# Performance work log

Measured on AMD Instinct MI355X. Metric: run time of the kernel, lower is better.

Reference implementation:

```python
import jax, jax.numpy as jnp
import numpy as np

ROPE_BASE = 10000.0

def _rope_tables(T, head_dim, dtype):
    inv_freq = 1.0 / (ROPE_BASE ** (jnp.arange(0, head_dim, 2, dtype=jnp.float32) / head_dim))
    t = jnp.arange(T, dtype=jnp.float32)
    freqs = jnp.einsum('t,f->tf', t, inv_freq)          # [T, head_dim/2]
    emb = jnp.concatenate([freqs, freqs], axis=-1)       # [T, head_dim]
    return jnp.sin(emb).astype(dtype), jnp.cos(emb).astype(dtype)

def _rotate_half(x):
    d = x.shape[-1] // 2
    return jnp.concatenate([-x[..., d:], x[..., :d]], axis=-1)

def _apply_rotary(x, sin, cos):
    # x: [B,H,T,hd]; sin/cos: [T,hd] broadcast over B,H
    return x * cos + _rotate_half(x) * sin

def setup_inputs() -> dict:
    key = jax.random.key(0)
    k1, k2, k3 = jax.random.split(key, 3)
    B, T, E = 2, 2048, 2048
    x = jax.random.normal(k1, (B, T, E), dtype=jnp.float32)
    attention_mask = jnp.ones((B, T), dtype=jnp.int32)
    W_qkv = jax.random.normal(k2, (E, 3 * E), dtype=jnp.float32) * (E ** -0.5)
    W_proj = jax.random.normal(k3, (E, E), dtype=jnp.float32) * (E ** -0.5)
    return {"x": x, "attention_mask": attention_mask, "W_qkv": W_qkv, "W_proj": W_proj}

def reference(x, attention_mask, W_qkv, W_proj):
    B, T, E = x.shape
    H = 16
    hd = E // H
    qkv = (x @ W_qkv).reshape(B, T, 3, H, hd)
    q, k, v = (jnp.moveaxis(qkv[:, :, i], 1, 2) for i in range(3))  # each [B,H,T,hd]
    sin, cos = _rope_tables(T, hd, x.dtype)
    q = _apply_rotary(q, sin, cos)
    k = _apply_rotary(k, sin, cos)
    # mask: True = masked out (causal future, padded keys, padded queries)
    causal = jnp.triu(jnp.ones((T, T), dtype=bool), 1)[None, None]      # [1,1,T,T]
    pad_k = (attention_mask == 0)[:, None, None, :]                     # [B,1,1,T]
    pad_q = (attention_mask == 0)[:, None, :, None]                     # [B,1,T,1]
    mask = causal | pad_k | pad_q                                       # [B,1,T,T]
    scale = hd ** -0.5
    scores = jnp.einsum('bhqd,bhkd->bhqk', q, k) * scale
    scores = jnp.where(mask, jnp.asarray(-1e9, scores.dtype), scores)
    attn = jax.nn.softmax(scores, axis=-1)
    out = jnp.einsum('bhqk,bhkd->bhqd', attn, v)                        # [B,H,T,hd]
    out = jnp.moveaxis(out, 1, 2).reshape(B, T, E)
    return out @ W_proj
```

## Files before the change

kernel.cpp:

```cpp
#include <hip/hip_runtime.h>
#include <math.h>

#define TT 2048
#define EE 2048
#define NH 16
#define HD 128
#define MM 4096
#define GK 2048

using f32x4  = __attribute__((ext_vector_type(4))) float;
using bf16x8 = __attribute__((ext_vector_type(8))) short;

#define MFMA16(a, b, c) __builtin_amdgcn_mfma_f32_16x16x32_bf16(a, b, c, 0, 0, 0)

__device__ __forceinline__ ushort bf_hi(float x) {
    uint u = __float_as_uint(x);
    uint r = (u + 0x7fffu + ((u >> 16) & 1u)) >> 16;
    return (ushort)r;
}
__device__ __forceinline__ float bf_f(ushort h) {
    return __uint_as_float(((uint)h) << 16);
}

__device__ __forceinline__ void gload16(const void* g, void* l) {
    __builtin_amdgcn_global_load_lds((const __attribute__((address_space(1))) void*)g,
                                     (__attribute__((address_space(3))) void*)l, 16, 0, 0);
}


template <int MODE>
__global__ __launch_bounds__(256)
void gemm_k(const float* __restrict__ A, const float* __restrict__ B,
            float* __restrict__ o0, float* __restrict__ o1, float* __restrict__ o2,
            int M, int N, int K)
{
    __shared__ float As[16][132];
    __shared__ float Bs[16][132];

    const int tid = threadIdx.x;
    const int tx = tid & 15;
    const int ty = tid >> 4;
    const int bm = blockIdx.y * 128;
    const int bn = blockIdx.x * 128;

    const int arow = tid >> 2;
    const int acq  = (tid & 3) << 2;
    const int brow = tid >> 5;
    const int bcol = (tid & 31) << 2;

    const float* Aptr = A + (size_t)(bm + arow) * K + acq;
    const float* Bptr = B + (size_t)brow * N + bn + bcol;

    float acc[8][8];
#pragma unroll
    for (int i = 0; i < 8; ++i)
#pragma unroll
        for (int j = 0; j < 8; ++j) acc[i][j] = 0.f;

    for (int kt = 0; kt < K; kt += 16) {
        float4 a0 = *(const float4*)(Aptr + kt);
        float4 a1 = *(const float4*)(Aptr + kt + (size_t)64 * K);
        float4 b0 = *(const float4*)(Bptr + (size_t)kt * N);
        float4 b1 = *(const float4*)(Bptr + (size_t)(kt + 8) * N);
        __syncthreads();
        As[acq + 0][arow] = a0.x; As[acq + 1][arow] = a0.y;
        As[acq + 2][arow] = a0.z; As[acq + 3][arow] = a0.w;
        As[acq + 0][arow + 64] = a1.x; As[acq + 1][arow + 64] = a1.y;
        As[acq + 2][arow + 64] = a1.z; As[acq + 3][arow + 64] = a1.w;
        *(float4*)&Bs[brow][bcol]     = b0;
        *(float4*)&Bs[brow + 8][bcol] = b1;
        __syncthreads();
#pragma unroll
        for (int kk = 0; kk < 16; ++kk) {
            float4 a_0 = *(const float4*)&As[kk][ty * 8];
            float4 a_1 = *(const float4*)&As[kk][ty * 8 + 4];
            float4 b_0 = *(const float4*)&Bs[kk][tx * 4];
            float4 b_1 = *(const float4*)&Bs[kk][tx * 4 + 64];
            float ar[8] = {a_0.x, a_0.y, a_0.z, a_0.w, a_1.x, a_1.y, a_1.z, a_1.w};
            float br[8] = {b_0.x, b_0.y, b_0.z, b_0.w, b_1.x, b_1.y, b_1.z, b_1.w};
#pragma unroll
            for (int i = 0; i < 8; ++i)
#pragma unroll
                for (int j = 0; j < 8; ++j)
                    acc[i][j] = fmaf(ar[i], br[j], acc[i][j]);
        }
    }

    if (MODE == 0) {
#pragma unroll
        for (int i = 0; i < 8; ++i) {
            size_t rowoff = (size_t)(bm + ty * 8 + i) * N + bn;
            *(float4*)&o0[rowoff + tx * 4]      = make_float4(acc[i][0], acc[i][1], acc[i][2], acc[i][3]);
            *(float4*)&o0[rowoff + 64 + tx * 4] = make_float4(acc[i][4], acc[i][5], acc[i][6], acc[i][7]);
        }
    } else {
        const int sel = bn >> 11;
        const int h   = (bn & 2047) >> 7;
        float* dst = (sel == 0) ? o0 : ((sel == 1) ? o1 : o2);
#pragma unroll
        for (int i = 0; i < 8; ++i) {
            int m = bm + ty * 8 + i;
            int b = m >> 11;
            int t = m & 2047;
            size_t base = (((size_t)b * NH + h) * TT + t) * HD;
            *(float4*)&dst[base + tx * 4]      = make_float4(acc[i][0], acc[i][1], acc[i][2], acc[i][3]);
            *(float4*)&dst[base + 64 + tx * 4] = make_float4(acc[i][4], acc[i][5], acc[i][6], acc[i][7]);
        }
    }
}

__global__ __launch_bounds__(256)
void split_x(const float* __restrict__ x, ushort* __restrict__ xh,
             ushort* __restrict__ xl)
{
    int idx = (blockIdx.x * 256 + threadIdx.x) * 4;
    float4 v = *(const float4*)&x[idx];
    float f[4] = {v.x, v.y, v.z, v.w};
    ushort h[4], l[4];
#pragma unroll
    for (int e = 0; e < 4; ++e) {
        h[e] = bf_hi(f[e]);
        l[e] = bf_hi(f[e] - bf_f(h[e]));
    }
    *(ushort4*)&xh[idx] = make_ushort4(h[0], h[1], h[2], h[3]);
    *(ushort4*)&xl[idx] = make_ushort4(l[0], l[1], l[2], l[3]);
}

__global__ __launch_bounds__(256)
void tw_prep(const float* __restrict__ W, int ldw, int c0,
             ushort* __restrict__ th, ushort* __restrict__ tl)
{
    __shared__ float tile[32][33];
    const int k0 = blockIdx.x * 32, n0 = blockIdx.y * 32;
    const int tx = threadIdx.x & 31, ty = threadIdx.x >> 5;
#pragma unroll
    for (int j = 0; j < 4; ++j)
        tile[ty + 8 * j][tx] = W[(size_t)(k0 + ty + 8 * j) * ldw + c0 + n0 + tx];
    __syncthreads();
#pragma unroll
    for (int j = 0; j < 4; ++j) {
        float v = tile[tx][ty + 8 * j];
        ushort h = bf_hi(v);
        ushort l = bf_hi(v - bf_f(h));
        size_t off = (size_t)(n0 + ty + 8 * j) * GK + k0 + tx;
        th[off] = h;
        tl[off] = l;
    }
}

template <int SCATTER>
__global__ __launch_bounds__(256)
void gemm_bf16(const ushort* __restrict__ Ah, const ushort* __restrict__ Al,
               const ushort* __restrict__ Bh, const ushort* __restrict__ Bl,
               float* __restrict__ out)
{
    __shared__ ushort AhS[4096], AlS[4096], BhS[4096], BlS[4096];

    const int tid  = threadIdx.x;
    const int wid  = tid >> 6;
    const int lane = tid & 63;
    const int lh   = lane >> 4;
    const int j16  = lane & 15;
    const int wm   = wid >> 1, wn = wid & 1;
    const int bm   = blockIdx.y * 128, bn = blockIdx.x * 128;

    const int g0 = wid * 128 + lane;
    const int g1 = g0 + 64;
    const int r0 = g0 >> 2, o0 = (g0 & 3) ^ (r0 & 3);
    const int r1 = g1 >> 2, o1 = (g1 & 3) ^ (r1 & 3);
    const size_t sa0 = (size_t)(bm + r0) * GK + o0 * 8;
    const size_t sa1 = (size_t)(bm + r1) * GK + o1 * 8;
    const size_t sb0 = (size_t)(bn + r0) * GK + o0 * 8;
    const size_t sb1 = (size_t)(bn + r1) * GK + o1 * 8;
    const ushort* a0h = Ah + sa0; const ushort* a1h = Ah + sa1;
    const ushort* a0l = Al + sa0; const ushort* a1l = Al + sa1;
    const ushort* b0h = Bh + sb0; const ushort* b1h = Bh + sb1;
    const ushort* b0l = Bl + sb0; const ushort* b1l = Bl + sb1;
    const int lds0 = wid * 1024;
    const int lds1 = wid * 1024 + 512;

    const int swz = (lh ^ (j16 & 3)) * 8;
    int offA[4], offB[4];
#pragma unroll
    for (int i = 0; i < 4; ++i) {
        offA[i] = (wm * 64 + i * 16 + j16) * 32 + swz;
        offB[i] = (wn * 64 + i * 16 + j16) * 32 + swz;
    }

    f32x4 acc[4][4];
#pragma unroll
    for (int i = 0; i < 4; ++i)
#pragma unroll
        for (int j = 0; j < 4; ++j)
#pragma unroll
            for (int e = 0; e < 4; ++e) acc[i][j][e] = 0.f;

    for (int kt = 0; kt < GK; kt += 32) {
        __syncthreads();
        gload16(a0h + kt, &AhS[lds0]);
        gload16(a1h + kt, &AhS[lds1]);
        gload16(a0l + kt, &AlS[lds0]);
        gload16(a1l + kt, &AlS[lds1]);
        gload16(b0h + kt, &BhS[lds0]);
        gload16(b1h + kt, &BhS[lds1]);
        gload16(b0l + kt, &BlS[lds0]);
        gload16(b1l + kt, &BlS[lds1]);
        __syncthreads();

        bf16x8 ah[4], al[4], bh[4], bl[4];
#pragma unroll
        for (int i = 0; i < 4; ++i) {
            ah[i] = *(const bf16x8*)&AhS[offA[i]];
            al[i] = *(const bf16x8*)&AlS[offA[i]];
            bh[i] = *(const bf16x8*)&BhS[offB[i]];
            bl[i] = *(const bf16x8*)&BlS[offB[i]];
        }
#pragma unroll
        for (int i = 0; i < 4; ++i)
#pragma unroll
            for (int j = 0; j < 4; ++j) {
                acc[i][j] = MFMA16(ah[i], bh[j], acc[i][j]);
                acc[i][j] = MFMA16(ah[i], bl[j], acc[i][j]);
                acc[i][j] = MFMA16(al[i], bh[j], acc[i][j]);
            }
    }

#pragma unroll
    for (int i = 0; i < 4; ++i)
#pragma unroll
        for (int j = 0; j < 4; ++j) {
            const int n = bn + wn * 64 + j * 16 + j16;
#pragma unroll
            for (int e = 0; e < 4; ++e) {
                const int m = bm + wm * 64 + i * 16 + 4 * lh + e;
                if (SCATTER) {
                    const int h = n >> 7, d = n & 127;
                    const int b = m >> 11, t = m & 2047;
                    out[(((size_t)b * NH + h) * TT + t) * HD + d] = acc[i][j][e];
                } else {
                    out[(size_t)m * EE + n] = acc[i][j][e];
                }
            }
        }
}

__global__ __launch_bounds__(256)
void rope_kernel(float* __restrict__ q, float* __restrict__ k)
{
    int idx = blockIdx.x * 256 + threadIdx.x;
    int j = idx & 63;
    int row = idx >> 6;
    int t = row & (TT - 1);
    float inv = __expf((float)(2 * j) * (-9.210340371976184f / 128.0f));
    float ang = (float)t * inv;
    float s, c;
    sincosf(ang, &s, &c);
    size_t base = (size_t)row * HD;
    float q0 = q[base + j], q1 = q[base + j + 64];
    q[base + j]      = q0 * c - q1 * s;
    q[base + j + 64] = q1 * c + q0 * s;
    float k0 = k[base + j], k1 = k[base + j + 64];
    k[base + j]      = k0 * c - k1 * s;
    k[base + j + 64] = k1 * c + k0 * s;
}

__global__ __launch_bounds__(256)
void transpose_v(const float* __restrict__ v, float* __restrict__ vt)
{
    __shared__ float tile[32][33];
    const int bh = blockIdx.z;
    const int t0 = blockIdx.x * 32, d0 = blockIdx.y * 32;
    const int tx = threadIdx.x & 31, ty = threadIdx.x >> 5;
#pragma unroll
    for (int j = 0; j < 4; ++j)
        tile[ty + 8 * j][tx] = v[((size_t)bh * TT + t0 + ty + 8 * j) * HD + d0 + tx];
    __syncthreads();
#pragma unroll
    for (int j = 0; j < 4; ++j)
        vt[((size_t)bh * HD + d0 + ty + 8 * j) * TT + t0 + tx] = tile[tx][ty + 8 * j];
}

template <int OM>
__global__ __launch_bounds__(256, 2)
void attn_mfma(const float* __restrict__ Q, const float* __restrict__ K,
               const float* __restrict__ Vt, const int* __restrict__ am,
               float* __restrict__ outF, ushort* __restrict__ oh,
               ushort* __restrict__ ol)
{
    __shared__ ushort KsH[32 * 128], KsL[32 * 128];
    __shared__ ushort VtH[128 * 32], VtL[128 * 32];
    __shared__ ushort PH[4][512], PL[4][512];
    __shared__ float  cor[4][16], lsum[4][16];

    const int tid  = threadIdx.x;
    const int wid  = tid >> 6;
    const int lane = tid & 63;
    const int lh   = lane >> 4;
    const int j16  = lane & 15;

    const int qt = (int)gridDim.x - 1 - (int)blockIdx.x;
    const int bh = blockIdx.y;
    const int bb = bh >> 4, hh = bh & 15;
    const int q0 = qt * 64;
    const int ntiles = 2 * qt + 2;

    const float scale = 0.08838834764831843f;
    bf16x8 qhf[4], qlf[4];
    {
        const float* qrow = Q + ((size_t)bh * TT + q0 + wid * 16 + j16) * HD;
#pragma unroll
        for (int kc = 0; kc < 4; ++kc) {
            float4 a = *(const float4*)(qrow + kc * 32 + lh * 8);
            float4 b = *(const float4*)(qrow + kc * 32 + lh * 8 + 4);
            float f[8] = {a.x, a.y, a.z, a.w, b.x, b.y, b.z, b.w};
#pragma unroll
            for (int e = 0; e < 8; ++e) {
                float x = f[e] * scale;
                ushort hv = bf_hi(x);
                ushort lv = bf_hi(x - bf_f(hv));
                qhf[kc][e] = (short)hv;
                qlf[kc][e] = (short)lv;
            }
        }
    }
    int qm[4];
#pragma unroll
    for (int r = 0; r < 4; ++r)
        qm[r] = am[bb * TT + q0 + wid * 16 + 4 * lh + r];

    float m_run[4] = {-3e38f, -3e38f, -3e38f, -3e38f};
    float l_run[4] = {0.f, 0.f, 0.f, 0.f};
    f32x4 acc_o[8];
#pragma unroll
    for (int dt = 0; dt < 8; ++dt)
#pragma unroll
        for (int e = 0; e < 4; ++e) acc_o[dt][e] = 0.f;

    for (int kt = 0; kt < ntiles; ++kt) {
        const int kv0 = kt * 32;
        const int km0 = am[bb * TT + kv0 + j16];
        const int km1 = am[bb * TT + kv0 + 16 + j16];

        __syncthreads();

        {
            const int kr = tid >> 3, f = tid & 7;
            const float* kp = K + ((size_t)bh * TT + kv0 + kr) * HD + f * 16;
            float4 f0 = *(const float4*)(kp + 0);
            float4 f1 = *(const float4*)(kp + 4);
            float4 f2 = *(const float4*)(kp + 8);
            float4 f3 = *(const float4*)(kp + 12);
            float fv[16] = {f0.x, f0.y, f0.z, f0.w, f1.x, f1.y, f1.z, f1.w,
                            f2.x, f2.y, f2.z, f2.w, f3.x, f3.y, f3.z, f3.w};
            ushort hs[16], lo_[16];
#pragma unroll
            for (int e = 0; e < 16; ++e) {
                ushort hv = bf_hi(fv[e]);
                hs[e] = hv;
                lo_[e] = bf_hi(fv[e] - bf_f(hv));
            }
            const int s0 = (2 * f) ^ (kr & 7);
            const int s1 = (2 * f + 1) ^ (kr & 7);
            uint4 wh0, wh1, wl0, wl1;
            wh0.x = hs[0] | ((uint)hs[1] << 16);  wh0.y = hs[2] | ((uint)hs[3] << 16);
            wh0.z = hs[4] | ((uint)hs[5] << 16);  wh0.w = hs[6] | ((uint)hs[7] << 16);
            wh1.x = hs[8] | ((uint)hs[9] << 16);  wh1.y = hs[10] | ((uint)hs[11] << 16);
            wh1.z = hs[12] | ((uint)hs[13] << 16); wh1.w = hs[14] | ((uint)hs[15] << 16);
            wl0.x = lo_[0] | ((uint)lo_[1] << 16);  wl0.y = lo_[2] | ((uint)lo_[3] << 16);
            wl0.z = lo_[4] | ((uint)lo_[5] << 16);  wl0.w = lo_[6] | ((uint)lo_[7] << 16);
            wl1.x = lo_[8] | ((uint)lo_[9] << 16);  wl1.y = lo_[10] | ((uint)lo_[11] << 16);
            wl1.z = lo_[12] | ((uint)lo_[13] << 16); wl1.w = lo_[14] | ((uint)lo_[15] << 16);
            *(uint4*)&KsH[kr * 128 + s0 * 8] = wh0;
            *(uint4*)&KsH[kr * 128 + s1 * 8] = wh1;
            *(uint4*)&KsL[kr * 128 + s0 * 8] = wl0;
            *(uint4*)&KsL[kr * 128 + s1 * 8] = wl1;
        }
        {
            const int f = tid & 7;
#pragma unroll
            for (int rr = 0; rr < 4; ++rr) {
                const int d = rr * 32 + (tid >> 3);
                const float* vp = Vt + ((size_t)bh * HD + d) * TT + kv0 + f * 4;
                float4 fv = *(const float4*)vp;
                float vals[4] = {fv.x, fv.y, fv.z, fv.w};
                ushort h4[4], l4[4];
#pragma unroll
                for (int e = 0; e < 4; ++e) {
                    ushort hv = bf_hi(vals[e]);
                    h4[e] = hv;
                    l4[e] = bf_hi(vals[e] - bf_f(hv));
                }
                const int sl = ((f >> 1) ^ ((d >> 1) & 3));
                const int off = d * 32 + sl * 8 + (f & 1) * 4;
                uint2 wh, wl;
                wh.x = h4[0] | ((uint)h4[1] << 16);  wh.y = h4[2] | ((uint)h4[3] << 16);
                wl.x = l4[0] | ((uint)l4[1] << 16);  wl.y = l4[2] | ((uint)l4[3] << 16);
                *(uint2*)&VtH[off] = wh;
                *(uint2*)&VtL[off] = wl;
            }
        }
        __syncthreads();

        f32x4 s0v, s1v;
#pragma unroll
        for (int e = 0; e < 4; ++e) { s0v[e] = 0.f; s1v[e] = 0.f; }
#pragma unroll
        for (int kc = 0; kc < 4; ++kc) {
            const int sA = (((kc * 4 + lh) ^ (j16 & 7)) * 8);
            bf16x8 kh0 = *(const bf16x8*)&KsH[j16 * 128 + sA];
            bf16x8 kl0 = *(const bf16x8*)&KsL[j16 * 128 + sA];
            bf16x8 kh1 = *(const bf16x8*)&KsH[(16 + j16) * 128 + sA];
            bf16x8 kl1 = *(const bf16x8*)&KsL[(16 + j16) * 128 + sA];
            s0v = MFMA16(qhf[kc], kh0, s0v);
            s0v = MFMA16(qhf[kc], kl0, s0v);
            s0v = MFMA16(qlf[kc], kh0, s0v);
            s1v = MFMA16(qhf[kc], kh1, s1v);
            s1v = MFMA16(qhf[kc], kl1, s1v);
            s1v = MFMA16(qlf[kc], kh1, s1v);
        }

        float p0[4], p1[4], corr[4];
#pragma unroll
        for (int r = 0; r < 4; ++r) {
            const int qg = q0 + wid * 16 + 4 * lh + r;
            float x0 = s0v[r], x1 = s1v[r];
            if ((kv0 + j16 > qg) | (km0 == 0) | (qm[r] == 0)) x0 = -1e9f;
            if ((kv0 + 16 + j16 > qg) | (km1 == 0) | (qm[r] == 0)) x1 = -1e9f;
            float rmax = fmaxf(x0, x1);
            rmax = fmaxf(rmax, __shfl_xor(rmax, 1));
            rmax = fmaxf(rmax, __shfl_xor(rmax, 2));
            rmax = fmaxf(rmax, __shfl_xor(rmax, 4));
            rmax = fmaxf(rmax, __shfl_xor(rmax, 8));
            float mnew = fmaxf(m_run[r], rmax);
            corr[r] = __expf(m_run[r] - mnew);
            m_run[r] = mnew;
            p0[r] = __expf(x0 - mnew);
            p1[r] = __expf(x1 - mnew);
            float ps = p0[r] + p1[r];
            ps += __shfl_xor(ps, 1);
            ps += __shfl_xor(ps, 2);
            ps += __shfl_xor(ps, 4);
            ps += __shfl_xor(ps, 8);
            l_run[r] = l_run[r] * corr[r] + ps;
        }

#pragma unroll
        for (int r = 0; r < 4; ++r) {
            const int q = 4 * lh + r;
            const int sw = (q >> 1) & 3;
            ushort h0 = bf_hi(p0[r]); ushort l0 = bf_hi(p0[r] - bf_f(h0));
            ushort h1 = bf_hi(p1[r]); ushort l1 = bf_hi(p1[r] - bf_f(h1));
            const int off0 = q * 32 + (((j16 >> 3) ^ sw) * 8) + (j16 & 7);
            const int off1 = q * 32 + ((((j16 >> 3) + 2) ^ sw) * 8) + (j16 & 7);
            PH[wid][off0] = h0; PL[wid][off0] = l0;
            PH[wid][off1] = h1; PL[wid][off1] = l1;
        }
        if (j16 == 0) {
            cor[wid][4 * lh + 0] = corr[0];
            cor[wid][4 * lh + 1] = corr[1];
            cor[wid][4 * lh + 2] = corr[2];
            cor[wid][4 * lh + 3] = corr[3];
        }

        const float cq = cor[wid][j16];
#pragma unroll
        for (int dt = 0; dt < 8; ++dt)
#pragma unroll
            for (int e = 0; e < 4; ++e) acc_o[dt][e] *= cq;

        const int sP = ((lh ^ ((j16 >> 1) & 3)) * 8);
        bf16x8 pbh = *(const bf16x8*)&PH[wid][j16 * 32 + sP];
        bf16x8 pbl = *(const bf16x8*)&PL[wid][j16 * 32 + sP];
#pragma unroll
        for (int dt = 0; dt < 8; ++dt) {
            const int d = dt * 16 + j16;
            const int sV = ((lh ^ ((d >> 1) & 3)) * 8);
            bf16x8 vh = *(const bf16x8*)&VtH[d * 32 + sV];
            bf16x8 vl = *(const bf16x8*)&VtL[d * 32 + sV];
            acc_o[dt] = MFMA16(vh, pbh, acc_o[dt]);
            acc_o[dt] = MFMA16(vh, pbl, acc_o[dt]);
            acc_o[dt] = MFMA16(vl, pbh, acc_o[dt]);
        }
    }

    if (j16 == 0) {
        lsum[wid][4 * lh + 0] = l_run[0];
        lsum[wid][4 * lh + 1] = l_run[1];
        lsum[wid][4 * lh + 2] = l_run[2];
        lsum[wid][4 * lh + 3] = l_run[3];
    }
    const float linv = 1.f / lsum[wid][j16];
    const int qg = q0 + wid * 16 + j16;
    const size_t obase = ((size_t)bb * TT + qg) * EE + hh * HD;
#pragma unroll
    for (int dt = 0; dt < 8; ++dt) {
        if (OM == 0) {
            outF[obase + dt * 16 + 4 * lh + 0] = acc_o[dt][0] * linv;
            outF[obase + dt * 16 + 4 * lh + 1] = acc_o[dt][1] * linv;
            outF[obase + dt * 16 + 4 * lh + 2] = acc_o[dt][2] * linv;
            outF[obase + dt * 16 + 4 * lh + 3] = acc_o[dt][3] * linv;
        } else {
            ushort h[4], l[4];
#pragma unroll
            for (int e = 0; e < 4; ++e) {
                float v = acc_o[dt][e] * linv;
                h[e] = bf_hi(v);
                l[e] = bf_hi(v - bf_f(h[e]));
            }
            *(ushort4*)&oh[obase + dt * 16 + 4 * lh] = make_ushort4(h[0], h[1], h[2], h[3]);
            *(ushort4*)&ol[obase + dt * 16 + 4 * lh] = make_ushort4(l[0], l[1], l[2], l[3]);
        }
    }
}

extern "C" void kernel_launch(void* const* d_in, const int* in_sizes, int n_in,
                              void* d_out, int out_size, void* d_ws, size_t ws_size,
                              hipStream_t stream)
{
    (void)in_sizes; (void)n_in; (void)out_size;
    const float* x     = (const float*)d_in[0];
    const int*   amask = (const int*)d_in[1];
    const float* Wqkv  = (const float*)d_in[2];
    const float* Wproj = (const float*)d_in[3];
    float* out = (float*)d_out;

    char* ws = (char*)d_ws;
    const size_t MB = 1024 * 1024;
    float* q = (float*)(ws + 0 * MB);
    float* k = (float*)(ws + 32 * MB);
    float* v = (float*)(ws + 64 * MB);

    if (ws_size >= 144 * MB) {
        ushort* ah  = (ushort*)(ws + 64 * MB);
        ushort* al  = (ushort*)(ws + 80 * MB);
        ushort* xh  = (ushort*)(ws + 96 * MB);
        ushort* xl  = (ushort*)(ws + 112 * MB);
        float*  vt  = (float*)(ws + 96 * MB);
        ushort* wth = (ushort*)(ws + 128 * MB);
        ushort* wtl = (ushort*)(ws + 136 * MB);

        split_x<<<(MM * EE) / (256 * 4), 256, 0, stream>>>(x, xh, xl);

        float* qkv[3] = {q, k, v};
        for (int s = 0; s < 3; ++s) {
            tw_prep<<<dim3(GK / 32, EE / 32), 256, 0, stream>>>(
                Wqkv, 3 * EE, s * EE, wth, wtl);
            gemm_bf16<1><<<dim3(EE / 128, MM / 128), 256, 0, stream>>>(
                xh, xl, wth, wtl, qkv[s]);
        }

        rope_kernel<<<(MM * NH * 64) / 256, 256, 0, stream>>>(q, k);

        transpose_v<<<dim3(TT / 32, HD / 32, 2 * NH), 256, 0, stream>>>(v, vt);

        tw_prep<<<dim3(GK / 32, EE / 32), 256, 0, stream>>>(
            Wproj, EE, 0, wth, wtl);

        attn_mfma<1><<<dim3(32, 2 * NH), 256, 0, stream>>>(
            q, k, vt, amask, nullptr, ah, al);

        gemm_bf16<0><<<dim3(EE / 128, MM / 128), 256, 0, stream>>>(
            ah, al, wth, wtl, out);
    } else {
        float* vt   = (float*)(ws + 96 * MB);
        float* attn = v;
        gemm_k<1><<<dim3(6144 / 128, MM / 128), 256, 0, stream>>>(
            x, Wqkv, q, k, v, MM, 3 * EE, EE);
        rope_kernel<<<(MM * NH * 64) / 256, 256, 0, stream>>>(q, k);
        transpose_v<<<dim3(TT / 32, HD / 32, 2 * NH), 256, 0, stream>>>(v, vt);
        attn_mfma<0><<<dim3(32, 2 * NH), 256, 0, stream>>>(
            q, k, vt, amask, attn, nullptr, nullptr);
        gemm_k<0><<<dim3(EE / 128, MM / 128), 256, 0, stream>>>(
            attn, Wproj, out, nullptr, nullptr, MM, EE, EE);
    }
}
```

Before: 1.031 ms.

## Pre-split K/V to bf16 pairs and enlarge attention tiles to 128x64

```diff
diff --git a/kernel.cpp b/kernel.cpp
--- a/kernel.cpp
+++ b/kernel.cpp
@@ -25,88 +25,6 @@
 __device__ __forceinline__ void gload16(const void* g, void* l) {
     __builtin_amdgcn_global_load_lds((const __attribute__((address_space(1))) void*)g,
                                      (__attribute__((address_space(3))) void*)l, 16, 0, 0);
-}
-
-
-template <int MODE>
-__global__ __launch_bounds__(256)
-void gemm_k(const float* __restrict__ A, const float* __restrict__ B,
-            float* __restrict__ o0, float* __restrict__ o1, float* __restrict__ o2,
-            int M, int N, int K)
-{
-    __shared__ float As[16][132];
-    __shared__ float Bs[16][132];
-
-    const int tid = threadIdx.x;
-    const int tx = tid & 15;
-    const int ty = tid >> 4;
-    const int bm = blockIdx.y * 128;
-    const int bn = blockIdx.x * 128;
-
-    const int arow = tid >> 2;
-    const int acq  = (tid & 3) << 2;
-    const int brow = tid >> 5;
-    const int bcol = (tid & 31) << 2;
-
-    const float* Aptr = A + (size_t)(bm + arow) * K + acq;
-    const float* Bptr = B + (size_t)brow * N + bn + bcol;
-
-    float acc[8][8];
-#pragma unroll
-    for (int i = 0; i < 8; ++i)
-#pragma unroll
-        for (int j = 0; j < 8; ++j) acc[i][j] = 0.f;
-
-    for (int kt = 0; kt < K; kt += 16) {
-        float4 a0 = *(const float4*)(Aptr + kt);
-        float4 a1 = *(const float4*)(Aptr + kt + (size_t)64 * K);
-        float4 b0 = *(const float4*)(Bptr + (size_t)kt * N);
-        float4 b1 = *(const float4*)(Bptr + (size_t)(kt + 8) * N);
-        __syncthreads();
-        As[acq + 0][arow] = a0.x; As[acq + 1][arow] = a0.y;
-        As[acq + 2][arow] = a0.z; As[acq + 3][arow] = a0.w;
-        As[acq + 0][arow + 64] = a1.x; As[acq + 1][arow + 64] = a1.y;
-        As[acq + 2][arow + 64] = a1.z; As[acq + 3][arow + 64] = a1.w;
-        *(float4*)&Bs[brow][bcol]     = b0;
-        *(float4*)&Bs[brow + 8][bcol] = b1;
-        __syncthreads();
-#pragma unroll
-        for (int kk = 0; kk < 16; ++kk) {
-            float4 a_0 = *(const float4*)&As[kk][ty * 8];
-            float4 a_1 = *(const float4*)&As[kk][ty * 8 + 4];
-            float4 b_0 = *(const float4*)&Bs[kk][tx * 4];
-            float4 b_1 = *(const float4*)&Bs[kk][tx * 4 + 64];
-            float ar[8] = {a_0.x, a_0.y, a_0.z, a_0.w, a_1.x, a_1.y, a_1.z, a_1.w};
-            float br[8] = {b_0.x, b_0.y, b_0.z, b_0.w, b_1.x, b_1.y, b_1.z, b_1.w};
-#pragma unroll
-            for (int i = 0; i < 8; ++i)
-#pragma unroll
-                for (int j = 0; j < 8; ++j)
-                    acc[i][j] = fmaf(ar[i], br[j], acc[i][j]);
-        }
-    }
-
-    if (MODE == 0) {
-#pragma unroll
-        for (int i = 0; i < 8; ++i) {
-            size_t rowoff = (size_t)(bm + ty * 8 + i) * N + bn;
-            *(float4*)&o0[rowoff + tx * 4]      = make_float4(acc[i][0], acc[i][1], acc[i][2], acc[i][3]);
-            *(float4*)&o0[rowoff + 64 + tx * 4] = make_float4(acc[i][4], acc[i][5], acc[i][6], acc[i][7]);
-        }
-    } else {
-        const int sel = bn >> 11;
-        const int h   = (bn & 2047) >> 7;
-        float* dst = (sel == 0) ? o0 : ((sel == 1) ? o1 : o2);
-#pragma unroll
-        for (int i = 0; i < 8; ++i) {
-            int m = bm + ty * 8 + i;
-            int b = m >> 11;
-            int t = m & 2047;
-            size_t base = (((size_t)b * NH + h) * TT + t) * HD;
-            *(float4*)&dst[base + tx * 4]      = make_float4(acc[i][0], acc[i][1], acc[i][2], acc[i][3]);
-            *(float4*)&dst[base + 64 + tx * 4] = make_float4(acc[i][4], acc[i][5], acc[i][6], acc[i][7]);
-        }
-    }
 }
 
 __global__ __launch_bounds__(256)
@@ -245,7 +163,8 @@
 }
 
 __global__ __launch_bounds__(256)
-void rope_kernel(float* __restrict__ q, float* __restrict__ k)
+void rope_split(float* __restrict__ q, const float* __restrict__ k,
+                ushort* __restrict__ kh, ushort* __restrict__ kl)
 {
     int idx = blockIdx.x * 256 + threadIdx.x;
     int j = idx & 63;
@@ -260,12 +179,16 @@
     q[base + j]      = q0 * c - q1 * s;
     q[base + j + 64] = q1 * c + q0 * s;
     float k0 = k[base + j], k1 = k[base + j + 64];
-    k[base + j]      = k0 * c - k1 * s;
-    k[base + j + 64] = k1 * c + k0 * s;
+    float ka = k0 * c - k1 * s;
+    float kb = k1 * c + k0 * s;
+    ushort ha = bf_hi(ka), hb = bf_hi(kb);
+    kh[base + j]      = ha;  kl[base + j]      = bf_hi(ka - bf_f(ha));
+    kh[base + j + 64] = hb;  kl[base + j + 64] = bf_hi(kb - bf_f(hb));
 }
 
 __global__ __launch_bounds__(256)
-void transpose_v(const float* __restrict__ v, float* __restrict__ vt)
+void transpose_split(const float* __restrict__ v, ushort* __restrict__ vth,
+                     ushort* __restrict__ vtl)
 {
     __shared__ float tile[32][33];
     const int bh = blockIdx.z;
@@ -276,21 +199,27 @@
         tile[ty + 8 * j][tx] = v[((size_t)bh * TT + t0 + ty + 8 * j) * HD + d0 + tx];
     __syncthreads();
 #pragma unroll
-    for (int j = 0; j < 4; ++j)
-        vt[((size_t)bh * HD + d0 + ty + 8 * j) * TT + t0 + tx] = tile[tx][ty + 8 * j];
-}
-
-template <int OM>
+    for (int j = 0; j < 4; ++j) {
+        float val = tile[tx][ty + 8 * j];
+        size_t off = ((size_t)bh * HD + d0 + ty + 8 * j) * TT + t0 + tx;
+        ushort h = bf_hi(val);
+        vth[off] = h;
+        vtl[off] = bf_hi(val - bf_f(h));
+    }
+}
+
 __global__ __launch_bounds__(256, 2)
-void attn_mfma(const float* __restrict__ Q, const float* __restrict__ K,
-               const float* __restrict__ Vt, const int* __restrict__ am,
-               float* __restrict__ outF, ushort* __restrict__ oh,
-               ushort* __restrict__ ol)
-{
-    __shared__ ushort KsH[32 * 128], KsL[32 * 128];
-    __shared__ ushort VtH[128 * 32], VtL[128 * 32];
-    __shared__ ushort PH[4][512], PL[4][512];
-    __shared__ float  cor[4][16], lsum[4][16];
+void attn_mfma2(const float* __restrict__ Q,
+                const ushort* __restrict__ KH, const ushort* __restrict__ KL,
+                const ushort* __restrict__ VH, const ushort* __restrict__ VL,
+                const int* __restrict__ am,
+                ushort* __restrict__ oh, ushort* __restrict__ ol)
+{
+    __shared__ ushort KhS[8192];
+    __shared__ ushort KlS[8192];
+    __shared__ ushort VhS[8192];
+    __shared__ ushort VlS[8192];
+    __shared__ float  cor[4][32], lsum[4][32];
 
     const int tid  = threadIdx.x;
     const int wid  = tid >> 6;
@@ -301,13 +230,26 @@
     const int qt = (int)gridDim.x - 1 - (int)blockIdx.x;
     const int bh = blockIdx.y;
     const int bb = bh >> 4, hh = bh & 15;
-    const int q0 = qt * 64;
+    const int q0 = qt * 128;
     const int ntiles = 2 * qt + 2;
 
+    int krow[4], kgl[4], vrow[4], vgl[4];
+#pragma unroll
+    for (int j = 0; j < 4; ++j) {
+        int p = wid * 256 + j * 64 + lane;
+        krow[j] = p >> 4; kgl[j] = (p & 15) ^ (krow[j] & 7);
+        vrow[j] = p >> 3; vgl[j] = (p & 7)  ^ (vrow[j] & 7);
+    }
+    const ushort* KHb = KH + (size_t)bh * TT * HD;
+    const ushort* KLb = KL + (size_t)bh * TT * HD;
+    const ushort* VHb = VH + (size_t)bh * HD * TT;
+    const ushort* VLb = VL + (size_t)bh * HD * TT;
+
     const float scale = 0.08838834764831843f;
-    bf16x8 qhf[4], qlf[4];
-    {
-        const float* qrow = Q + ((size_t)bh * TT + q0 + wid * 16 + j16) * HD;
+    bf16x8 qhf[2][4], qlf[2][4];
+#pragma unroll
+    for (int g = 0; g < 2; ++g) {
+        const float* qrow = Q + ((size_t)bh * TT + q0 + wid * 32 + g * 16 + j16) * HD;
 #pragma unroll
         for (int kc = 0; kc < 4; ++kc) {
             float4 a = *(const float4*)(qrow + kc * 32 + lh * 8);
@@ -318,197 +260,190 @@
                 float x = f[e] * scale;
                 ushort hv = bf_hi(x);
                 ushort lv = bf_hi(x - bf_f(hv));
-                qhf[kc][e] = (short)hv;
-                qlf[kc][e] = (short)lv;
-            }
-        }
-    }
-    int qm[4];
-#pragma unroll
-    for (int r = 0; r < 4; ++r)
-        qm[r] = am[bb * TT + q0 + wid * 16 + 4 * lh + r];
-
-    float m_run[4] = {-3e38f, -3e38f, -3e38f, -3e38f};
-    float l_run[4] = {0.f, 0.f, 0.f, 0.f};
-    f32x4 acc_o[8];
+                qhf[g][kc][e] = (short)hv;
+                qlf[g][kc][e] = (short)lv;
+            }
+        }
+    }
+    int qmk[2][4];
+#pragma unroll
+    for (int g = 0; g < 2; ++g)
+#pragma unroll
+        for (int r = 0; r < 4; ++r)
+            qmk[g][r] = am[bb * TT + q0 + wid * 32 + g * 16 + 4 * lh + r];
+
+    float m_run[2][4], l_run[2][4];
+#pragma unroll
+    for (int g = 0; g < 2; ++g)
+#pragma unroll
+        for (int r = 0; r < 4; ++r) { m_run[g][r] = -3e38f; l_run[g][r] = 0.f; }
+    f32x4 acc[8][2];
 #pragma unroll
     for (int dt = 0; dt < 8; ++dt)
 #pragma unroll
-        for (int e = 0; e < 4; ++e) acc_o[dt][e] = 0.f;
+        for (int cg = 0; cg < 2; ++cg)
+#pragma unroll
+            for (int e = 0; e < 4; ++e) acc[dt][cg][e] = 0.f;
+
+    ushort* PH = &KhS[wid * 2048];
+    ushort* PL = &KlS[wid * 2048];
 
     for (int kt = 0; kt < ntiles; ++kt) {
-        const int kv0 = kt * 32;
-        const int km0 = am[bb * TT + kv0 + j16];
-        const int km1 = am[bb * TT + kv0 + 16 + j16];
-
+        const int kv0 = kt * 64;
+        int km[4];
+#pragma unroll
+        for (int kg = 0; kg < 4; ++kg)
+            km[kg] = am[bb * TT + kv0 + kg * 16 + j16];
+
+#pragma unroll
+        for (int j = 0; j < 4; ++j) {
+            const int gb = (wid * 256 + j * 64) * 8;
+            gload16(KHb + (size_t)(kv0 + krow[j]) * HD + kgl[j] * 8, &KhS[gb]);
+            gload16(KLb + (size_t)(kv0 + krow[j]) * HD + kgl[j] * 8, &KlS[gb]);
+            gload16(VHb + (size_t)vrow[j] * TT + kv0 + vgl[j] * 8,   &VhS[gb]);
+            gload16(VLb + (size_t)vrow[j] * TT + kv0 + vgl[j] * 8,   &VlS[gb]);
+        }
         __syncthreads();
 
-        {
-            const int kr = tid >> 3, f = tid & 7;
-            const float* kp = K + ((size_t)bh * TT + kv0 + kr) * HD + f * 16;
-            float4 f0 = *(const float4*)(kp + 0);
-            float4 f1 = *(const float4*)(kp + 4);
-            float4 f2 = *(const float4*)(kp + 8);
-            float4 f3 = *(const float4*)(kp + 12);
-            float fv[16] = {f0.x, f0.y, f0.z, f0.w, f1.x, f1.y, f1.z, f1.w,
-                            f2.x, f2.y, f2.z, f2.w, f3.x, f3.y, f3.z, f3.w};
-            ushort hs[16], lo_[16];
-#pragma unroll
-            for (int e = 0; e < 16; ++e) {
-                ushort hv = bf_hi(fv[e]);
-                hs[e] = hv;
-                lo_[e] = bf_hi(fv[e] - bf_f(hv));
-            }
-            const int s0 = (2 * f) ^ (kr & 7);
-            const int s1 = (2 * f + 1) ^ (kr & 7);
-            uint4 wh0, wh1, wl0, wl1;
-            wh0.x = hs[0] | ((uint)hs[1] << 16);  wh0.y = hs[2] | ((uint)hs[3] << 16);
-            wh0.z = hs[4] | ((uint)hs[5] << 16);  wh0.w = hs[6] | ((uint)hs[7] << 16);
-            wh1.x = hs[8] | ((uint)hs[9] << 16);  wh1.y = hs[10] | ((uint)hs[11] << 16);
-            wh1.z = hs[12] | ((uint)hs[13] << 16); wh1.w = hs[14] | ((uint)hs[15] << 16);
-            wl0.x = lo_[0] | ((uint)lo_[1] << 16);  wl0.y = lo_[2] | ((uint)lo_[3] << 16);
-            wl0.z = lo_[4] | ((uint)lo_[5] << 16);  wl0.w = lo_[6] | ((uint)lo_[7] << 16);
-            wl1.x = lo_[8] | ((uint)lo_[9] << 16);  wl1.y = lo_[10] | ((uint)lo_[11] << 16);
-            wl1.z = lo_[12] | ((uint)lo_[13] << 16); wl1.w = lo_[14] | ((uint)lo_[15] << 16);
-            *(uint4*)&KsH[kr * 128 + s0 * 8] = wh0;
-            *(uint4*)&KsH[kr * 128 + s1 * 8] = wh1;
-            *(uint4*)&KsL[kr * 128 + s0 * 8] = wl0;
-            *(uint4*)&KsL[kr * 128 + s1 * 8] = wl1;
-        }
-        {
-            const int f = tid & 7;
-#pragma unroll
-            for (int rr = 0; rr < 4; ++rr) {
-                const int d = rr * 32 + (tid >> 3);
-                const float* vp = Vt + ((size_t)bh * HD + d) * TT + kv0 + f * 4;
-                float4 fv = *(const float4*)vp;
-                float vals[4] = {fv.x, fv.y, fv.z, fv.w};
-                ushort h4[4], l4[4];
-#pragma unroll
-                for (int e = 0; e < 4; ++e) {
-                    ushort hv = bf_hi(vals[e]);
-                    h4[e] = hv;
-                    l4[e] = bf_hi(vals[e] - bf_f(hv));
+        f32x4 s[2][4];
+#pragma unroll
+        for (int g = 0; g < 2; ++g)
+#pragma unroll
+            for (int kg = 0; kg < 4; ++kg)
+#pragma unroll
+                for (int e = 0; e < 4; ++e) s[g][kg][e] = 0.f;
+#pragma unroll
+        for (int kc = 0; kc < 4; ++kc) {
+#pragma unroll
+            for (int kg = 0; kg < 4; ++kg) {
+                const int idx = (kg * 16 + j16) * 128 + (((kc * 4 + lh) ^ (j16 & 7)) * 8);
+                bf16x8 kh = *(const bf16x8*)&KhS[idx];
+                bf16x8 kl = *(const bf16x8*)&KlS[idx];
+#pragma unroll
+                for (int g = 0; g < 2; ++g) {
+                    s[g][kg] = MFMA16(qhf[g][kc], kh, s[g][kg]);
+                    s[g][kg] = MFMA16(qhf[g][kc], kl, s[g][kg]);
+                    s[g][kg] = MFMA16(qlf[g][kc], kh, s[g][kg]);
                 }
-                const int sl = ((f >> 1) ^ ((d >> 1) & 3));
-                const int off = d * 32 + sl * 8 + (f & 1) * 4;
-                uint2 wh, wl;
-                wh.x = h4[0] | ((uint)h4[1] << 16);  wh.y = h4[2] | ((uint)h4[3] << 16);
-                wl.x = l4[0] | ((uint)l4[1] << 16);  wl.y = l4[2] | ((uint)l4[3] << 16);
-                *(uint2*)&VtH[off] = wh;
-                *(uint2*)&VtL[off] = wl;
-            }
-        }
+            }
+        }
+
+        float pv[2][4][4], corr[2][4];
+#pragma unroll
+        for (int g = 0; g < 2; ++g)
+#pragma unroll
+            for (int r = 0; r < 4; ++r) {
+                const int qg = q0 + wid * 32 + g * 16 + 4 * lh + r;
+                float x[4];
+                float tmax = -3e38f;
+#pragma unroll
+                for (int kg = 0; kg < 4; ++kg) {
+                    const int key = kv0 + kg * 16 + j16;
+                    float xx = s[g][kg][r];
+                    if ((key > qg) | (km[kg] == 0) | (qmk[g][r] == 0)) xx = -1e9f;
+                    x[kg] = xx;
+                    tmax = fmaxf(tmax, xx);
+                }
+                tmax = fmaxf(tmax, __shfl_xor(tmax, 1));
+                tmax = fmaxf(tmax, __shfl_xor(tmax, 2));
+                tmax = fmaxf(tmax, __shfl_xor(tmax, 4));
+                tmax = fmaxf(tmax, __shfl_xor(tmax, 8));
+                float mnew = fmaxf(m_run[g][r], tmax);
+                corr[g][r] = __expf(m_run[g][r] - mnew);
+                m_run[g][r] = mnew;
+                float psum = 0.f;
+#pragma unroll
+                for (int kg = 0; kg < 4; ++kg) {
+                    pv[g][r][kg] = __expf(x[kg] - mnew);
+                    psum += pv[g][r][kg];
+                }
+                psum += __shfl_xor(psum, 1);
+                psum += __shfl_xor(psum, 2);
+                psum += __shfl_xor(psum, 4);
+                psum += __shfl_xor(psum, 8);
+                l_run[g][r] = l_run[g][r] * corr[g][r] + psum;
+                if (j16 == 0) cor[wid][g * 16 + 4 * lh + r] = corr[g][r];
+            }
+
         __syncthreads();
 
-        f32x4 s0v, s1v;
-#pragma unroll
-        for (int e = 0; e < 4; ++e) { s0v[e] = 0.f; s1v[e] = 0.f; }
-#pragma unroll
-        for (int kc = 0; kc < 4; ++kc) {
-            const int sA = (((kc * 4 + lh) ^ (j16 & 7)) * 8);
-            bf16x8 kh0 = *(const bf16x8*)&KsH[j16 * 128 + sA];
-            bf16x8 kl0 = *(const bf16x8*)&KsL[j16 * 128 + sA];
-            bf16x8 kh1 = *(const bf16x8*)&KsH[(16 + j16) * 128 + sA];
-            bf16x8 kl1 = *(const bf16x8*)&KsL[(16 + j16) * 128 + sA];
-            s0v = MFMA16(qhf[kc], kh0, s0v);
-            s0v = MFMA16(qhf[kc], kl0, s0v);
-            s0v = MFMA16(qlf[kc], kh0, s0v);
-            s1v = MFMA16(qhf[kc], kh1, s1v);
-            s1v = MFMA16(qhf[kc], kl1, s1v);
-            s1v = MFMA16(qlf[kc], kh1, s1v);
-        }
-
-        float p0[4], p1[4], corr[4];
-#pragma unroll
-        for (int r = 0; r < 4; ++r) {
-            const int qg = q0 + wid * 16 + 4 * lh + r;
-            float x0 = s0v[r], x1 = s1v[r];
-            if ((kv0 + j16 > qg) | (km0 == 0) | (qm[r] == 0)) x0 = -1e9f;
-            if ((kv0 + 16 + j16 > qg) | (km1 == 0) | (qm[r] == 0)) x1 = -1e9f;
-            float rmax = fmaxf(x0, x1);
-            rmax = fmaxf(rmax, __shfl_xor(rmax, 1));
-            rmax = fmaxf(rmax, __shfl_xor(rmax, 2));
-            rmax = fmaxf(rmax, __shfl_xor(rmax, 4));
-            rmax = fmaxf(rmax, __shfl_xor(rmax, 8));
-            float mnew = fmaxf(m_run[r], rmax);
-            corr[r] = __expf(m_run[r] - mnew);
-            m_run[r] = mnew;
-            p0[r] = __expf(x0 - mnew);
-            p1[r] = __expf(x1 - mnew);
-            float ps = p0[r] + p1[r];
-            ps += __shfl_xor(ps, 1);
-            ps += __shfl_xor(ps, 2);
-            ps += __shfl_xor(ps, 4);
-            ps += __shfl_xor(ps, 8);
-            l_run[r] = l_run[r] * corr[r] + ps;
-        }
-
-#pragma unroll
-        for (int r = 0; r < 4; ++r) {
-            const int q = 4 * lh + r;
-            const int sw = (q >> 1) & 3;
-            ushort h0 = bf_hi(p0[r]); ushort l0 = bf_hi(p0[r] - bf_f(h0));
-            ushort h1 = bf_hi(p1[r]); ushort l1 = bf_hi(p1[r] - bf_f(h1));
-            const int off0 = q * 32 + (((j16 >> 3) ^ sw) * 8) + (j16 & 7);
-            const int off1 = q * 32 + ((((j16 >> 3) + 2) ^ sw) * 8) + (j16 & 7);
-            PH[wid][off0] = h0; PL[wid][off0] = l0;
-            PH[wid][off1] = h1; PL[wid][off1] = l1;
-        }
-        if (j16 == 0) {
-            cor[wid][4 * lh + 0] = corr[0];
-            cor[wid][4 * lh + 1] = corr[1];
-            cor[wid][4 * lh + 2] = corr[2];
-            cor[wid][4 * lh + 3] = corr[3];
-        }
-
-        const float cq = cor[wid][j16];
+#pragma unroll
+        for (int g = 0; g < 2; ++g)
+#pragma unroll
+            for (int r = 0; r < 4; ++r) {
+                const int q = g * 16 + 4 * lh + r;
+#pragma unroll
+                for (int kg = 0; kg < 4; ++kg) {
+                    const int glog = kg * 2 + (j16 >> 3);
+                    const int idx = q * 64 + ((glog ^ (q & 7)) * 8) + (j16 & 7);
+                    float p = pv[g][r][kg];
+                    ushort h = bf_hi(p);
+                    PH[idx] = h;
+                    PL[idx] = bf_hi(p - bf_f(h));
+                }
+            }
+
+        const float cq0 = cor[wid][j16];
+        const float cq1 = cor[wid][16 + j16];
 #pragma unroll
         for (int dt = 0; dt < 8; ++dt)
 #pragma unroll
-            for (int e = 0; e < 4; ++e) acc_o[dt][e] *= cq;
-
-        const int sP = ((lh ^ ((j16 >> 1) & 3)) * 8);
-        bf16x8 pbh = *(const bf16x8*)&PH[wid][j16 * 32 + sP];
-        bf16x8 pbl = *(const bf16x8*)&PL[wid][j16 * 32 + sP];
+            for (int e = 0; e < 4; ++e) {
+                acc[dt][0][e] *= cq0;
+                acc[dt][1][e] *= cq1;
+            }
+
+#pragma unroll
+        for (int c = 0; c < 2; ++c) {
+            bf16x8 pbh0, pbl0, pbh1, pbl1;
+            {
+                const int p0 = (j16) * 64 + (((c * 4 + lh) ^ (j16 & 7)) * 8);
+                const int p1 = (16 + j16) * 64 + (((c * 4 + lh) ^ (j16 & 7)) * 8);
+                pbh0 = *(const bf16x8*)&PH[p0];
+                pbl0 = *(const bf16x8*)&PL[p0];
+                pbh1 = *(const bf16x8*)&PH[p1];
+                pbl1 = *(const bf16x8*)&PL[p1];
+            }
+#pragma unroll
+            for (int dt = 0; dt < 8; ++dt) {
+                const int vidx = (dt * 16 + j16) * 64 + (((c * 4 + lh) ^ (j16 & 7)) * 8);
+                bf16x8 vh = *(const bf16x8*)&VhS[vidx];
+                bf16x8 vl = *(const bf16x8*)&VlS[vidx];
+                acc[dt][0] = MFMA16(vh, pbh0, acc[dt][0]);
+                acc[dt][0] = MFMA16(vh, pbl0, acc[dt][0]);
+                acc[dt][0] = MFMA16(vl, pbh0, acc[dt][0]);
+                acc[dt][1] = MFMA16(vh, pbh1, acc[dt][1]);
+                acc[dt][1] = MFMA16(vh, pbl1, acc[dt][1]);
+                acc[dt][1] = MFMA16(vl, pbh1, acc[dt][1]);
+            }
+        }
+        __syncthreads();
+    }
+
+    if (j16 == 0) {
+#pragma unroll
+        for (int g = 0; g < 2; ++g)
+#pragma unroll
+            for (int r = 0; r < 4; ++r)
+                lsum[wid][g * 16 + 4 * lh + r] = l_run[g][r];
+    }
+#pragma unroll
+    for (int cg = 0; cg < 2; ++cg) {
+        const float lv = lsum[wid][cg * 16 + j16];
+        const float linv = (lv > 0.f) ? (1.f / lv) : 0.f;
+        const int qg = q0 + wid * 32 + cg * 16 + j16;
+        const size_t ob = ((size_t)bb * TT + qg) * EE + hh * HD;
 #pragma unroll
         for (int dt = 0; dt < 8; ++dt) {
-            const int d = dt * 16 + j16;
-            const int sV = ((lh ^ ((d >> 1) & 3)) * 8);
-            bf16x8 vh = *(const bf16x8*)&VtH[d * 32 + sV];
-            bf16x8 vl = *(const bf16x8*)&VtL[d * 32 + sV];
-            acc_o[dt] = MFMA16(vh, pbh, acc_o[dt]);
-            acc_o[dt] = MFMA16(vh, pbl, acc_o[dt]);
-            acc_o[dt] = MFMA16(vl, pbh, acc_o[dt]);
-        }
-    }
-
-    if (j16 == 0) {
-        lsum[wid][4 * lh + 0] = l_run[0];
-        lsum[wid][4 * lh + 1] = l_run[1];
-        lsum[wid][4 * lh + 2] = l_run[2];
-        lsum[wid][4 * lh + 3] = l_run[3];
-    }
-    const float linv = 1.f / lsum[wid][j16];
-    const int qg = q0 + wid * 16 + j16;
-    const size_t obase = ((size_t)bb * TT + qg) * EE + hh * HD;
-#pragma unroll
-    for (int dt = 0; dt < 8; ++dt) {
-        if (OM == 0) {
-            outF[obase + dt * 16 + 4 * lh + 0] = acc_o[dt][0] * linv;
-            outF[obase + dt * 16 + 4 * lh + 1] = acc_o[dt][1] * linv;
-            outF[obase + dt * 16 + 4 * lh + 2] = acc_o[dt][2] * linv;
-            outF[obase + dt * 16 + 4 * lh + 3] = acc_o[dt][3] * linv;
-        } else {
             ushort h[4], l[4];
 #pragma unroll
             for (int e = 0; e < 4; ++e) {
-                float v = acc_o[dt][e] * linv;
+                float v = acc[dt][cg][e] * linv;
                 h[e] = bf_hi(v);
                 l[e] = bf_hi(v - bf_f(h[e]));
             }
-            *(ushort4*)&oh[obase + dt * 16 + 4 * lh] = make_ushort4(h[0], h[1], h[2], h[3]);
-            *(ushort4*)&ol[obase + dt * 16 + 4 * lh] = make_ushort4(l[0], l[1], l[2], l[3]);
+            *(ushort4*)&oh[ob + dt * 16 + 4 * lh] = make_ushort4(h[0], h[1], h[2], h[3]);
+            *(ushort4*)&ol[ob + dt * 16 + 4 * lh] = make_ushort4(l[0], l[1], l[2], l[3]);
         }
     }
 }
@@ -517,7 +452,7 @@
                               void* d_out, int out_size, void* d_ws, size_t ws_size,
                               hipStream_t stream)
 {
-    (void)in_sizes; (void)n_in; (void)out_size;
+    (void)in_sizes; (void)n_in; (void)out_size; (void)ws_size;
     const float* x     = (const float*)d_in[0];
     const int*   amask = (const int*)d_in[1];
     const float* Wqkv  = (const float*)d_in[2];
@@ -526,51 +461,39 @@
 
     char* ws = (char*)d_ws;
     const size_t MB = 1024 * 1024;
-    float* q = (float*)(ws + 0 * MB);
-    float* k = (float*)(ws + 32 * MB);
-    float* v = (float*)(ws + 64 * MB);
-
-    if (ws_size >= 144 * MB) {
-        ushort* ah  = (ushort*)(ws + 64 * MB);
-        ushort* al  = (ushort*)(ws + 80 * MB);
-        ushort* xh  = (ushort*)(ws + 96 * MB);
-        ushort* xl  = (ushort*)(ws + 112 * MB);
-        float*  vt  = (float*)(ws + 96 * MB);
-        ushort* wth = (ushort*)(ws + 128 * MB);
-        ushort* wtl = (ushort*)(ws + 136 * MB);
-
-        split_x<<<(MM * EE) / (256 * 4), 256, 0, stream>>>(x, xh, xl);
-
-        float* qkv[3] = {q, k, v};
-        for (int s = 0; s < 3; ++s) {
-            tw_prep<<<dim3(GK / 32, EE / 32), 256, 0, stream>>>(
-                Wqkv, 3 * EE, s * EE, wth, wtl);
-            gemm_bf16<1><<<dim3(EE / 128, MM / 128), 256, 0, stream>>>(
-                xh, xl, wth, wtl, qkv[s]);
-        }
-
-        rope_kernel<<<(MM * NH * 64) / 256, 256, 0, stream>>>(q, k);
-
-        transpose_v<<<dim3(TT / 32, HD / 32, 2 * NH), 256, 0, stream>>>(v, vt);
-
+    float*  q   = (float*)(ws + 0 * MB);
+    float*  k   = (float*)(ws + 32 * MB);
+    float*  v   = (float*)(ws + 64 * MB);
+    ushort* vth = (ushort*)(ws + 32 * MB);
+    ushort* vtl = (ushort*)(ws + 48 * MB);
+    ushort* ah  = (ushort*)(ws + 64 * MB);
+    ushort* al  = (ushort*)(ws + 80 * MB);
+    ushort* xh  = (ushort*)(ws + 96 * MB);
+    ushort* xl  = (ushort*)(ws + 112 * MB);
+    ushort* kh  = (ushort*)(ws + 96 * MB);
+    ushort* kl  = (ushort*)(ws + 112 * MB);
+    ushort* wth = (ushort*)(ws + 128 * MB);
+    ushort* wtl = (ushort*)(ws + 136 * MB);
+
+    split_x<<<(MM * EE) / (256 * 4), 256, 0, stream>>>(x, xh, xl);
+
+    float* qkv[3] = {q, k, v};
+    for (int s = 0; s < 3; ++s) {
         tw_prep<<<dim3(GK / 32, EE / 32), 256, 0, stream>>>(
-            Wproj, EE, 0, wth, wtl);
-
-        attn_mfma<1><<<dim3(32, 2 * NH), 256, 0, stream>>>(
-            q, k, vt, amask, nullptr, ah, al);
-
-        gemm_bf16<0><<<dim3(EE / 128, MM / 128), 256, 0, stream>>>(
-            ah, al, wth, wtl, out);
-    } else {
-        float* vt   = (float*)(ws + 96 * MB);
-        float* attn = v;
-        gemm_k<1><<<dim3(6144 / 128, MM / 128), 256, 0, stream>>>(
-            x, Wqkv, q, k, v, MM, 3 * EE, EE);
-        rope_kernel<<<(MM * NH * 64) / 256, 256, 0, stream>>>(q, k);
-        transpose_v<<<dim3(TT / 32, HD / 32, 2 * NH), 256, 0, stream>>>(v, vt);
-        attn_mfma<0><<<dim3(32, 2 * NH), 256, 0, stream>>>(
-            q, k, vt, amask, attn, nullptr, nullptr);
-        gemm_k<0><<<dim3(EE / 128, MM / 128), 256, 0, stream>>>(
-            attn, Wproj, out, nullptr, nullptr, MM, EE, EE);
-    }
-}
+            Wqkv, 3 * EE, s * EE, wth, wtl);
+        gemm_bf16<1><<<dim3(EE / 128, MM / 128), 256, 0, stream>>>(
+            xh, xl, wth, wtl, qkv[s]);
+    }
+
+    rope_split<<<(MM * NH * 64) / 256, 256, 0, stream>>>(q, k, kh, kl);
+
+    transpose_split<<<dim3(TT / 32, HD / 32, 2 * NH), 256, 0, stream>>>(v, vth, vtl);
+
+    tw_prep<<<dim3(GK / 32, EE / 32), 256, 0, stream>>>(Wproj, EE, 0, wth, wtl);
+
+    attn_mfma2<<<dim3(TT / 128, 2 * NH), 256, 0, stream>>>(
+        q, kh, kl, vth, vtl, amask, ah, al);
+
+    gemm_bf16<0><<<dim3(EE / 128, MM / 128), 256, 0, stream>>>(
+        ah, al, wth, wtl, out);
+}
```

Result: slower. 1.385 ms (+34.4%).
